# Kernel optimization log

Measured on AMD Instinct MI355X. Metric: run time of the kernel, lower is better.

## Reference

```python
import math
import jax, jax.numpy as jnp
import numpy as np

D_MODEL = 512
H = 8          # head_num
HD = 64        # head_dim
ETA = 4
R = 8
D_FFC = 2048
EPS = 1e-6
GRU_BIAS = 2.0
T, B = 128, 32
TOTAL_PROJ = H * HD * 5 + H * ETA * 3  # 2656


def _layer_norm(x, g, b):
    m = x.mean(-1, keepdims=True)
    v = ((x - m) ** 2).mean(-1, keepdims=True)
    return (x - m) / jnp.sqrt(v + 1e-5) * g + b


def _outer(a, b):
    # a: (T,B,H,D), b: (T,B,H,E) -> (T,B,H,D*E), row-major over (D,E) like torch bmm+reshape
    t, bb, h, d = a.shape
    return (a[..., :, None] * b[..., None, :]).reshape(t, bb, h, d * b.shape[-1])


def _gru_gate(x, y, w, u):
    # GTrXL-style gating: x = residual stream, y = new signal. w,u: (3, d, d)
    r = jax.nn.sigmoid(y @ w[0].T + x @ u[0].T)
    z = jax.nn.sigmoid(y @ w[1].T + x @ u[1].T - GRU_BIAS)
    h = jnp.tanh(y @ w[2].T + (r * x) @ u[2].T)
    return (1.0 - z) * x + z * h


def _discounted_sum(prev, x, d):
    # y_t = d_t * y_{t-1} + x_t, y_{-1} = prev. x: (T, ...), d broadcastable to x.
    def step(c, xd):
        xi, di = xd
        nc = di * c + xi
        return nc, nc
    _, ys = jax.lax.scan(step, prev, (x, d))
    return ys


def setup_inputs() -> dict:
    key = jax.random.key(0)
    ks = jax.random.split(key, 12)
    sc_p = 1.0 / math.sqrt(D_MODEL)
    return {
        "inputs": jax.random.normal(ks[0], (T, B, D_MODEL), jnp.float32),
        "terminations": jax.random.randint(ks[1], (T, B), 0, 2).astype(jnp.int32),
        "tilde_k": jnp.zeros((B, R, H, ETA * HD), jnp.float32),
        "tilde_v": jnp.zeros((B, R, H, HD), jnp.float32),
        "s_prev": jnp.zeros((B, H, ETA * HD), jnp.float32),
        "tick": jnp.zeros((B, 1), jnp.float32),
        "w_proj": jax.random.normal(ks[2], (TOTAL_PROJ, D_MODEL), jnp.float32) * sc_p,
        "b_proj": jnp.zeros((TOTAL_PROJ,), jnp.float32),
        "w_attn": jax.random.normal(ks[3], (D_MODEL, H * HD), jnp.float32) * (1.0 / math.sqrt(H * HD)),
        "b_attn": jnp.zeros((D_MODEL,), jnp.float32),
        "ln1_g": jnp.ones((D_MODEL,), jnp.float32),
        "ln1_b": jnp.zeros((D_MODEL,), jnp.float32),
        "ln2_g": jnp.ones((D_MODEL,), jnp.float32),
        "ln2_b": jnp.zeros((D_MODEL,), jnp.float32),
        "gru1_w": jax.random.normal(ks[4], (3, D_MODEL, D_MODEL), jnp.float32) * sc_p,
        "gru1_u": jax.random.normal(ks[5], (3, D_MODEL, D_MODEL), jnp.float32) * sc_p,
        "gru2_w": jax.random.normal(ks[6], (3, D_MODEL, D_MODEL), jnp.float32) * sc_p,
        "gru2_u": jax.random.normal(ks[7], (3, D_MODEL, D_MODEL), jnp.float32) * sc_p,
        "ffc_w1": jax.random.normal(ks[8], (D_FFC, D_MODEL), jnp.float32) * sc_p,
        "ffc_b1": jnp.zeros((D_FFC,), jnp.float32),
        "ffc_w2": jax.random.normal(ks[9], (D_MODEL, D_FFC), jnp.float32) * (1.0 / math.sqrt(D_FFC)),
        "ffc_b2": jnp.zeros((D_MODEL,), jnp.float32),
    }


def _forward(inputs, terminations, tilde_k, tilde_v, s_prev, tick,
             w_proj, b_proj, w_attn, b_attn, ln1_g, ln1_b, ln2_g, ln2_b,
             gru1_w, gru1_u, gru2_w, gru2_u, ffc_w1, ffc_b1, ffc_w2, ffc_b2):
    t, bsz, _ = inputs.shape
    omegas = jnp.linspace(-math.pi, math.pi, R).astype(inputs.dtype)

    x_normed = _layer_norm(inputs, ln1_g, ln1_b)
    all_proj = x_normed @ w_proj.T + b_proj  # (T,B,2656)
    kqv_dim = H * HD * 5
    kqvbg = all_proj[..., :kqv_dim].reshape(t, bsz, H, 5, HD)
    p123 = all_proj[..., kqv_dim:].reshape(t, bsz, H, 3, ETA)

    keys = kqvbg[..., 0, :]
    queries = kqvbg[..., 1, :]
    values = kqvbg[..., 2, :]
    beta = jax.nn.sigmoid(kqvbg[..., 3, :])
    gammas = kqvbg[..., 4, :]
    p1, p2, p3 = p123[..., 0, :], p123[..., 1, :], p123[..., 2, :]

    keys_exp = _outer(jax.nn.relu(keys), jax.nn.relu(p1))          # (T,B,H,HD*ETA)
    queries_exp = _outer(jax.nn.relu(queries), jax.nn.relu(p2))
    gammas_exp = _outer(jax.nn.sigmoid(gammas), jax.nn.sigmoid(p3))

    ticks = tick[None] + jnp.arange(1, t + 1, dtype=tick.dtype).reshape(t, 1, 1)  # (T,B,1)
    occil = jnp.cos(ticks * omegas)  # (T,B,R)

    values_gated = values * beta                 # (T,B,H,HD)
    keys_gated = keys_exp * gammas_exp           # (T,B,H,HD*ETA)
    s_in = keys_gated
    values_osc = values_gated[:, :, None] * occil[..., None, None]  # (T,B,R,H,HD)
    keys_osc = keys_gated[:, :, None] * occil[..., None, None]      # (T,B,R,H,HD*ETA)

    term_mask = (1.0 - terminations.astype(inputs.dtype))[:, :, None, None]  # (T,B,1,1)
    discount_gamma = (1.0 - gammas_exp) * term_mask   # (T,B,H,HD*ETA)
    discount_beta = (1.0 - beta) * term_mask          # (T,B,H,HD)

    final_keys = _discounted_sum(tilde_k, keys_osc, discount_gamma[:, :, None])
    final_values = _discounted_sum(tilde_v, values_osc, discount_beta[:, :, None])
    final_s = _discounted_sum(s_prev, s_in, discount_gamma)

    kdq = (final_keys * queries_exp[:, :, None]).sum(-1)   # (T,B,R,H)
    kv = (final_values * kdq[..., None]).sum(2)             # (T,B,H,HD)
    norm = (final_s * queries_exp).sum(-1) + EPS            # (T,B,H)
    attn = kv / (2 * R * norm[..., None])
    attn = attn.reshape(t, bsz, H * HD) @ w_attn.T + b_attn  # (T,B,d_model)

    gating1 = _gru_gate(inputs, jax.nn.relu(attn), gru1_w, gru1_u)
    ffc_in = _layer_norm(gating1, ln2_g, ln2_b)
    ffc_out = jax.nn.relu(jax.nn.relu(ffc_in @ ffc_w1.T + ffc_b1) @ ffc_w2.T + ffc_b2)
    output = _gru_gate(gating1, ffc_out, gru2_w, gru2_u)
    return output


def reference(inputs, terminations, tilde_k, tilde_v, s_prev, tick,
              w_proj, b_proj, w_attn, b_attn, ln1_g, ln1_b, ln2_g, ln2_b,
              gru1_w, gru1_u, gru2_w, gru2_u, ffc_w1, ffc_b1, ffc_w2, ffc_b2):
    return _forward(inputs, terminations, tilde_k, tilde_v, s_prev, tick,
                    w_proj, b_proj, w_attn, b_attn, ln1_g, ln1_b, ln2_g, ln2_b,
                    gru1_w, gru1_u, gru2_w, gru2_u, ffc_w1, ffc_b1, ffc_w2, ffc_b2)
```

## Files before the change

### kernel.cpp

```cpp
#include <hip/hip_runtime.h>
#include <hip/hip_bf16.h>
#include <math.h>

#define DM   512
#define HH   8
#define RR   8
#define TT   128
#define BBATCH 32
#define MM   (TT*BBATCH)
#define NPROJ 2656
#define KQV  2560

typedef __attribute__((ext_vector_type(8))) short bf16x8;
typedef __attribute__((ext_vector_type(4))) float f32x4;

__device__ __forceinline__ float sigmoidf_(float x) {
    return 1.0f / (1.0f + __expf(-x));
}

__device__ __forceinline__ void gload_lds16(const void* g, void* l) {
    __builtin_amdgcn_global_load_lds(
        (const __attribute__((address_space(1))) unsigned int*)g,
        (__attribute__((address_space(3))) unsigned int*)l, 16, 0, 0);
}

template<int CTRL, int RMASK>
__device__ __forceinline__ float dpp_add_(float x) {
    union { float f; int i; } a, b;
    a.f = x;
    b.i = __builtin_amdgcn_update_dpp(0, a.i, CTRL, RMASK, 0xf, true);
    return x + b.f;
}
__device__ __forceinline__ float wave_sum_u(float x) {
    x = dpp_add_<0x111, 0xf>(x);
    x = dpp_add_<0x112, 0xf>(x);
    x = dpp_add_<0x114, 0xf>(x);
    x = dpp_add_<0x118, 0xf>(x);
    x = dpp_add_<0x142, 0xa>(x);
    x = dpp_add_<0x143, 0xc>(x);
    union { float f; int i; } s, t;
    s.f = x;
    t.i = __builtin_amdgcn_readlane(s.i, 63);
    return t.f;
}

struct F2B9 {
    const float* s[9];
    __hip_bfloat16* d[9];
    int cum[10];
};

__global__ __launch_bounds__(256) void f2b_ln_all(F2B9 a,
    const float* __restrict__ x, const float* __restrict__ g,
    const float* __restrict__ b, __hip_bfloat16* __restrict__ lnout)
{
    if (blockIdx.x < 8752) {
        int q = blockIdx.x * 256 + threadIdx.x;
        if (q >= a.cum[9]) return;
        int s = 0;
        #pragma unroll
        for (int i = 1; i < 9; ++i) s += (q >= a.cum[i]);
        int i4 = (q - a.cum[s]) * 4;
        float4 v = *(const float4*)(a.s[s] + i4);
        __hip_bfloat16* dst = a.d[s] + i4;
        dst[0] = __float2bfloat16(v.x);
        dst[1] = __float2bfloat16(v.y);
        dst[2] = __float2bfloat16(v.z);
        dst[3] = __float2bfloat16(v.w);
        return;
    }
    int row = blockIdx.x - 8752;
    int tid = threadIdx.x;
    const float* xr = x + (size_t)row * DM;
    float2 v = ((const float2*)xr)[tid];
    float s = v.x + v.y;
    #pragma unroll
    for (int off = 32; off; off >>= 1) s += __shfl_down(s, off);
    __shared__ float red[8];
    int wid = tid >> 6, lane = tid & 63;
    if (lane == 0) red[wid] = s;
    __syncthreads();
    if (tid == 0) red[0] = (red[0] + red[1] + red[2] + red[3]) * (1.0f / DM);
    __syncthreads();
    float mean = red[0];
    float dx = v.x - mean, dy = v.y - mean;
    float sq = dx*dx + dy*dy;
    #pragma unroll
    for (int off = 32; off; off >>= 1) sq += __shfl_down(sq, off);
    if (lane == 0) red[4 + wid] = sq;
    __syncthreads();
    if (tid == 0) red[1] = rsqrtf((red[4]+red[5]+red[6]+red[7]) * (1.0f/DM) + 1e-5f);
    __syncthreads();
    float rstd = red[1];
    float2 gg = ((const float2*)g)[tid];
    float2 bb = ((const float2*)b)[tid];
    __hip_bfloat16* orow = lnout + (size_t)row * DM;
    orow[2*tid+0] = __float2bfloat16(dx * rstd * gg.x + bb.x);
    orow[2*tid+1] = __float2bfloat16(dy * rstd * gg.y + bb.y);
}

__device__ __forceinline__ void gemm_core128(
    const __hip_bfloat16* __restrict__ A, const __hip_bfloat16* __restrict__ W,
    const float* __restrict__ bias,
    float* __restrict__ Cf, __hip_bfloat16* __restrict__ Cb,
    int N, int K, int act, int m0, int n0,
    __hip_bfloat16* As, __hip_bfloat16* Bs)
{
    int tid = threadIdx.x;
    int wave = tid >> 6, lane = tid & 63;
    int wm = (wave >> 1) * 64, wn = (wave & 1) * 64;
    int fr = lane & 15, fq = lane >> 4;

    f32x4 acc[4][4];
    #pragma unroll
    for (int i = 0; i < 4; ++i)
        #pragma unroll
        for (int j = 0; j < 4; ++j)
            acc[i][j] = (f32x4){0.f, 0.f, 0.f, 0.f};

    int sm0 = wave*16 + fr;
    int sm1 = sm0 + 64;
    int wr0 = n0 + sm0; if (wr0 >= N) wr0 = N - 1;
    int wr1 = n0 + sm1; if (wr1 >= N) wr1 = N - 1;
    const __hip_bfloat16* Ag0 = A + (size_t)(m0 + sm0) * K + fq*8;
    const __hip_bfloat16* Ag1 = A + (size_t)(m0 + sm1) * K + fq*8;
    const __hip_bfloat16* Wg0 = W + (size_t)wr0 * K + fq*8;
    const __hip_bfloat16* Wg1 = W + (size_t)wr1 * K + fq*8;

    for (int k0 = 0; k0 < K; k0 += 32) {
        gload_lds16(Ag0 + k0, As + (size_t)wave*512);
        gload_lds16(Ag1 + k0, As + (size_t)(wave+4)*512);
        gload_lds16(Wg0 + k0, Bs + (size_t)wave*512);
        gload_lds16(Wg1 + k0, Bs + (size_t)(wave+4)*512);
        __syncthreads();
        bf16x8 af[4], bfr[4];
        #pragma unroll
        for (int i = 0; i < 4; ++i) {
            af[i]  = *(const bf16x8*)(As + (size_t)(wm/16 + i)*512 + lane*8);
            bfr[i] = *(const bf16x8*)(Bs + (size_t)(wn/16 + i)*512 + lane*8);
        }
        #pragma unroll
        for (int mi = 0; mi < 4; ++mi)
            #pragma unroll
            for (int ni = 0; ni < 4; ++ni)
                acc[mi][ni] = __builtin_amdgcn_mfma_f32_16x16x32_bf16(
                    af[mi], bfr[ni], acc[mi][ni], 0, 0, 0);
        __syncthreads();
    }

    #pragma unroll
    for (int ni = 0; ni < 4; ++ni) {
        int n = n0 + wn + ni*16 + fr;
        bool nok = n < N;
        float bv = (bias && nok) ? bias[n] : 0.f;
        #pragma unroll
        for (int mi = 0; mi < 4; ++mi) {
            #pragma unroll
            for (int r = 0; r < 4; ++r) {
                int m = m0 + wm + mi*16 + fq*4 + r;
                float v = acc[mi][ni][r] + bv;
                if (act) v = fmaxf(v, 0.f);
                if (nok) {
                    size_t idx = (size_t)m * N + n;
                    if (Cf) Cf[idx] = v;
                    if (Cb) Cb[idx] = __float2bfloat16(v);
                }
            }
        }
    }
}

__global__ __launch_bounds__(256) void gemm_bf16(
    const __hip_bfloat16* __restrict__ A, const __hip_bfloat16* __restrict__ W,
    const float* __restrict__ bias,
    float* __restrict__ Cf, __hip_bfloat16* __restrict__ Cb,
    int N, int K, int act)
{
    __shared__ __attribute__((aligned(16))) __hip_bfloat16 As[8*512];
    __shared__ __attribute__((aligned(16))) __hip_bfloat16 Bs[8*512];
    gemm_core128(A, W, bias, Cf, Cb, N, K, act, blockIdx.y * 128, blockIdx.x * 128, As, Bs);
}

__global__ __launch_bounds__(256) void ffc1_bx_dual(
    const __hip_bfloat16* __restrict__ Aa, const __hip_bfloat16* __restrict__ Wa,
    const float* __restrict__ biasA, __hip_bfloat16* __restrict__ CbA,
    int Na, int splitX,
    const __hip_bfloat16* __restrict__ Ab, const __hip_bfloat16* __restrict__ Wb,
    float* __restrict__ CfB, int Nb, int K)
{
    __shared__ __attribute__((aligned(16))) __hip_bfloat16 As[8*512];
    __shared__ __attribute__((aligned(16))) __hip_bfloat16 Bs[8*512];
    int bx = blockIdx.x;
    if (bx < splitX)
        gemm_core128(Aa, Wa, biasA, nullptr, CbA, Na, K, 1, blockIdx.y*128, bx*128, As, Bs);
    else
        gemm_core128(Ab, Wb, nullptr, CfB, nullptr, Nb, K, 0, blockIdx.y*128, (bx-splitX)*128, As, Bs);
}

__global__ __launch_bounds__(256) void gemm_bf16_64(
    const __hip_bfloat16* __restrict__ A, const __hip_bfloat16* __restrict__ W,
    const float* __restrict__ bias,
    float* __restrict__ Cf, __hip_bfloat16* __restrict__ Cb,
    int N, int K, int act)
{
    __shared__ __attribute__((aligned(16))) __hip_bfloat16 As[4*512];
    __shared__ __attribute__((aligned(16))) __hip_bfloat16 Bs[8*512];
    int tid = threadIdx.x;
    int wave = tid >> 6, lane = tid & 63;
    int m0 = blockIdx.y * 64, n0 = blockIdx.x * 128;
    int wm = (wave >> 1) * 32, wn = (wave & 1) * 64;
    int fr = lane & 15, fq = lane >> 4;

    f32x4 acc[2][4];
    #pragma unroll
    for (int i = 0; i < 2; ++i)
        #pragma unroll
        for (int j = 0; j < 4; ++j)
            acc[i][j] = (f32x4){0.f, 0.f, 0.f, 0.f};

    const __hip_bfloat16* Ag = A + (size_t)(m0 + wave*16 + fr) * K + fq*8;
    int wr0 = n0 + wave*16 + fr; if (wr0 >= N) wr0 = N - 1;
    int wr1 = wr0 + 64;          if (wr1 >= N) wr1 = N - 1;
    const __hip_bfloat16* Wg0 = W + (size_t)wr0 * K + fq*8;
    const __hip_bfloat16* Wg1 = W + (size_t)wr1 * K + fq*8;

    for (int k0 = 0; k0 < K; k0 += 32) {
        gload_lds16(Ag  + k0, As + (size_t)wave*512);
        gload_lds16(Wg0 + k0, Bs + (size_t)wave*512);
        gload_lds16(Wg1 + k0, Bs + (size_t)(wave+4)*512);
        __syncthreads();
        bf16x8 af[2], bfr[4];
        #pragma unroll
        for (int i = 0; i < 2; ++i)
            af[i]  = *(const bf16x8*)(As + (size_t)(wm/16 + i)*512 + lane*8);
        #pragma unroll
        for (int j = 0; j < 4; ++j)
            bfr[j] = *(const bf16x8*)(Bs + (size_t)(wn/16 + j)*512 + lane*8);
        #pragma unroll
        for (int mi = 0; mi < 2; ++mi)
            #pragma unroll
            for (int ni = 0; ni < 4; ++ni)
                acc[mi][ni] = __builtin_amdgcn_mfma_f32_16x16x32_bf16(
                    af[mi], bfr[ni], acc[mi][ni], 0, 0, 0);
        __syncthreads();
    }

    #pragma unroll
    for (int ni = 0; ni < 4; ++ni) {
        int n = n0 + wn + ni*16 + fr;
        bool nok = n < N;
        float bv = (bias && nok) ? bias[n] : 0.f;
        #pragma unroll
        for (int mi = 0; mi < 2; ++mi) {
            #pragma unroll
            for (int r = 0; r < 4; ++r) {
                int m = m0 + wm + mi*16 + fq*4 + r;
                float v = acc[mi][ni][r] + bv;
                if (act) v = fmaxf(v, 0.f);
                if (nok) {
                    size_t idx = (size_t)m * N + n;
                    if (Cf) Cf[idx] = v;
                    if (Cb) Cb[idx] = __float2bfloat16(v);
                }
            }
        }
    }
}

#define NCH   4
#define CHK   32
#define BNDF  (44*64)

__global__ __launch_bounds__(256) void scan_attn_fused(
    const float* __restrict__ proj, const int* __restrict__ term,
    const float* __restrict__ tick, const float* __restrict__ tilde_k,
    const float* __restrict__ tilde_v, const float* __restrict__ s_prev,
    __hip_bfloat16* __restrict__ attn,
    const __hip_bfloat16* __restrict__ gA, const __hip_bfloat16* __restrict__ gW,
    float* __restrict__ gC)
{
    extern __shared__ __attribute__((aligned(16))) char smem_dyn[];
    int bid = blockIdx.x;
    if (bid >= 256) {
        __hip_bfloat16* As = (__hip_bfloat16*)smem_dyn;
        __hip_bfloat16* Bs = As + 8*512;
        int g = bid - 256;
        gemm_core128(gA, gW, nullptr, gC, nullptr, 1024, DM, 0,
                     (g >> 3) * 128, (g & 7) * 128, As, Bs);
        return;
    }

    float* bnd  = (float*)smem_dyn;
    float* occt = bnd + 3*BNDF;
    int*   flags= (int*)(occt + TT*8);

    const int b = bid >> 3, h = bid & 7;
    const int tid = threadIdx.x;
    const int wv = tid >> 6, lane = tid & 63;
    const int t0 = wv * CHK;

    const float tk = tick[b];
    if (tid < 4) flags[tid] = 0;
    {
        const float PI_ = 3.14159265358979323846f;
        #pragma unroll
        for (int i = 0; i < 4; ++i) {
            int idx = tid*4 + i;
            int t = idx >> 3, r = idx & 7;
            float w = -PI_ + (float)r * (2.0f*PI_/7.0f);
            occt[idx] = cosf((tk + (float)(t + 1)) * w);
        }
    }
    __syncthreads();

    int tmv = (lane < CHK) ? term[(size_t)(t0 + lane)*BBATCH + b] : 0;

    float fs[4], fk[8][4], fv[8], Pg[4], Pb;

    auto zero_state = [&]() {
        #pragma unroll
        for (int j = 0; j < 4; ++j) fs[j] = 0.f;
        #pragma unroll
        for (int r = 0; r < 8; ++r) {
            #pragma unroll
            for (int j = 0; j < 4; ++j) fk[r][j] = 0.f;
            fv[r] = 0.f;
        }
    };
    auto load_init = [&]() {
        float4 s4 = *(const float4*)(s_prev + ((size_t)(b*HH + h))*256 + lane*4);
        fs[0]=s4.x; fs[1]=s4.y; fs[2]=s4.z; fs[3]=s4.w;
        #pragma unroll
        for (int r = 0; r < 8; ++r) {
            float4 k4 = *(const float4*)(tilde_k + (((size_t)b*RR + r)*HH + h)*256 + lane*4);
            fk[r][0]=k4.x; fk[r][1]=k4.y; fk[r][2]=k4.z; fk[r][3]=k4.w;
            fv[r] = tilde_v[(((size_t)b*RR + r)*HH + h)*64 + lane];
        }
    };
    auto load_bnd = [&](int w) {
        const float* p = bnd + w*BNDF;
        #pragma unroll
        for (int j = 0; j < 4; ++j) fs[j] = p[j*64 + lane];
        #pragma unroll
        for (int r = 0; r < 8; ++r) {
            #pragma unroll
            for (int j = 0; j < 4; ++j) fk[r][j] = p[(4 + r*4 + j)*64 + lane];
            fv[r] = p[(36 + r)*64 + lane];
        }
    };
    auto store_bnd = [&](int w) {
        float* p = bnd + w*BNDF;
        #pragma unroll
        for (int j = 0; j < 4; ++j) p[j*64 + lane] = fs[j];
        #pragma unroll
        for (int r = 0; r < 8; ++r) {
            #pragma unroll
            for (int j = 0; j < 4; ++j) p[(4 + r*4 + j)*64 + lane] = fk[r][j];
            p[(36 + r)*64 + lane] = fv[r];
        }
    };
    auto combine = [&](int w) {
        const float* p = bnd + w*BNDF;
        #pragma unroll
        for (int j = 0; j < 4; ++j) fs[j] = fmaf(Pg[j], p[j*64 + lane], fs[j]);
        #pragma unroll
        for (int r = 0; r < 8; ++r) {
            #pragma unroll
            for (int j = 0; j < 4; ++j)
                fk[r][j] = fmaf(Pg[j], p[(4 + r*4 + j)*64 + lane], fk[r][j]);
            fv[r] = fmaf(Pb, p[(36 + r)*64 + lane], fv[r]);
        }
    };

    struct Raw { float k, q, v, be, ga; float4 P1, P2, P3; };
    auto load_raw = [&](int t, Raw& rw) {
        const float* prow = proj + (size_t)(t*BBATCH + b) * NPROJ;
        const float* p5 = prow + h*320;
        rw.k  = p5[lane];
        rw.q  = p5[64  + lane];
        rw.v  = p5[128 + lane];
        rw.be = p5[192 + lane];
        rw.ga = p5[256 + lane];
        const float* pp = prow + KQV + h*12;
        rw.P1 = *(const float4*)(pp);
        rw.P2 = *(const float4*)(pp + 4);
        rw.P3 = *(const float4*)(pp + 8);
    };

    auto sweep = [&](bool out) {
        Pg[0]=Pg[1]=Pg[2]=Pg[3]=1.f; Pb=1.f;
        Raw cur, nxt;
        load_raw(t0, cur);
        for (int i = 0; i < CHK; ++i) {
            const int t = t0 + i;
            if (i + 1 < CHK) load_raw(t + 1, nxt);
            const int tm = __builtin_amdgcn_readlane(tmv, i);
            const float mask = 1.0f - (float)tm;
            float kr = fmaxf(cur.k, 0.f);
            float sg = sigmoidf_(cur.ga);
            float sb = sigmoidf_(cur.be);
            float vg = cur.v * sb;
            float db = (1.f - sb) * mask;
            float p1a[4] = {cur.P1.x, cur.P1.y, cur.P1.z, cur.P1.w};
            float p3a[4] = {cur.P3.x, cur.P3.y, cur.P3.z, cur.P3.w};
            float kg[4], dg[4];
            #pragma unroll
            for (int j = 0; j < 4; ++j) {
                float gexp = sg * sigmoidf_(p3a[j]);
                kg[j] = kr * fmaxf(p1a[j], 0.f) * gexp;
                dg[j] = (1.f - gexp) * mask;
            }
            float occ[8];
            {
                float4 o0 = *(const float4*)(occt + t*8);
                float4 o1 = *(const float4*)(occt + t*8 + 4);
                occ[0]=o0.x; occ[1]=o0.y; occ[2]=o0.z; occ[3]=o0.w;
                occ[4]=o1.x; occ[5]=o1.y; occ[6]=o1.z; occ[7]=o1.w;
            }
            #pragma unroll
            for (int j = 0; j < 4; ++j) {
                fs[j] = fmaf(dg[j], fs[j], kg[j]);
                Pg[j] *= dg[j];
            }
            #pragma unroll
            for (int r = 0; r < 8; ++r) {
                #pragma unroll
                for (int j = 0; j < 4; ++j)
                    fk[r][j] = fmaf(dg[j], fk[r][j], kg[j]*occ[r]);
                fv[r] = fmaf(db, fv[r], vg*occ[r]);
            }
            Pb *= db;
            if (out) {
                float qr = fmaxf(cur.q, 0.f);
                float p2a[4] = {cur.P2.x, cur.P2.y, cur.P2.z, cur.P2.w};
                float qe[4];
                #pragma unroll
                for (int j = 0; j < 4; ++j) qe[j] = qr * fmaxf(p2a[j], 0.f);
                float snorm = fs[0]*qe[0] + fs[1]*qe[1] + fs[2]*qe[2] + fs[3]*qe[3];
                float nrm_u = wave_sum_u(snorm);
                float kdq_u[8];
                #pragma unroll
                for (int r = 0; r < 8; ++r) {
                    float kdq = fk[r][0]*qe[0] + fk[r][1]*qe[1]
                              + fk[r][2]*qe[2] + fk[r][3]*qe[3];
                    kdq_u[r] = wave_sum_u(kdq);
                }
                float kv = 0.f;
                #pragma unroll
                for (int r = 0; r < 8; ++r) kv = fmaf(fv[r], kdq_u[r], kv);
                attn[(size_t)(t*BBATCH + b)*DM + h*64 + lane] =
                    __float2bfloat16(kv / (16.f * (nrm_u + 1e-6f)));
            }
            cur = nxt;
        }
    };

    if (wv < NCH - 1) {
        if (wv == 0) load_init(); else zero_state();
        sweep(false);
        if (wv > 0) {
            while (__hip_atomic_load(&flags[wv-1], __ATOMIC_ACQUIRE,
                                     __HIP_MEMORY_SCOPE_WORKGROUP) == 0)
                __builtin_amdgcn_s_sleep(1);
            combine(wv - 1);
        }
        store_bnd(wv);
        if (lane == 0)
            __hip_atomic_store(&flags[wv], 1, __ATOMIC_RELEASE,
                               __HIP_MEMORY_SCOPE_WORKGROUP);
    }

    if (wv == 0) {
        load_init();
    } else {
        while (__hip_atomic_load(&flags[wv-1], __ATOMIC_ACQUIRE,
                                 __HIP_MEMORY_SCOPE_WORKGROUP) == 0)
            __builtin_amdgcn_s_sleep(1);
        load_bnd(wv - 1);
    }
    sweep(true);
}

__global__ __launch_bounds__(256) void gru_rz_kernel(const float* __restrict__ A1,
    const float* __restrict__ Bx, const float* __restrict__ x,
    __hip_bfloat16* __restrict__ rx, float* __restrict__ z)
{
    size_t i = (size_t)blockIdx.x * 256 + threadIdx.x;
    size_t m = i >> 9;
    int c = (int)(i & 511);
    float rpre = A1[m*1536 + c]       + Bx[m*1024 + c];
    float zpre = A1[m*1536 + 512 + c] + Bx[m*1024 + 512 + c] - 2.0f;
    rx[i] = __float2bfloat16(sigmoidf_(rpre) * x[i]);
    z[i]  = sigmoidf_(zpre);
}

__global__ __launch_bounds__(256) void gru_final_kernel(const float* __restrict__ A1,
    const float* __restrict__ C2, const float* __restrict__ z,
    const float* __restrict__ x, float* __restrict__ out)
{
    size_t i = (size_t)blockIdx.x * 256 + threadIdx.x;
    size_t m = i >> 9;
    int c = (int)(i & 511);
    float hh = tanhf(A1[m*1536 + 1024 + c] + C2[i]);
    float zz = z[i];
    out[i] = (1.0f - zz) * x[i] + zz * hh;
}

__global__ __launch_bounds__(256) void gru_final_ln(
    const float* __restrict__ A1, const float* __restrict__ C2,
    const float* __restrict__ z, const float* __restrict__ x,
    const float* __restrict__ g, const float* __restrict__ bta,
    float* __restrict__ g1, __hip_bfloat16* __restrict__ g1b,
    __hip_bfloat16* __restrict__ fib)
{
    int row = blockIdx.x;
    int tid = threadIdx.x;
    size_t base = (size_t)row * DM;
    float2 c2v = ((const float2*)(C2 + base))[tid];
    float2 zv  = ((const float2*)(z  + base))[tid];
    float2 xv  = ((const float2*)(x  + base))[tid];
    float2 av  = ((const float2*)(A1 + (size_t)row*1536 + 1024))[tid];
    float h0 = tanhf(av.x + c2v.x);
    float h1 = tanhf(av.y + c2v.y);
    float2 v;
    v.x = (1.0f - zv.x) * xv.x + zv.x * h0;
    v.y = (1.0f - zv.y) * xv.y + zv.y * h1;
    ((float2*)(g1 + base))[tid] = v;
    g1b[base + 2*tid+0] = __float2bfloat16(v.x);
    g1b[base + 2*tid+1] = __float2bfloat16(v.y);

    float s = v.x + v.y;
    #pragma unroll
    for (int off = 32; off; off >>= 1) s += __shfl_down(s, off);
    __shared__ float red[8];
    int wid = tid >> 6, lane = tid & 63;
    if (lane == 0) red[wid] = s;
    __syncthreads();
    if (tid == 0) red[0] = (red[0] + red[1] + red[2] + red[3]) * (1.0f / DM);
    __syncthreads();
    float mean = red[0];
    float dx = v.x - mean, dy = v.y - mean;
    float sq = dx*dx + dy*dy;
    #pragma unroll
    for (int off = 32; off; off >>= 1) sq += __shfl_down(sq, off);
    if (lane == 0) red[4 + wid] = sq;
    __syncthreads();
    if (tid == 0) red[1] = rsqrtf((red[4]+red[5]+red[6]+red[7]) * (1.0f/DM) + 1e-5f);
    __syncthreads();
    float rstd = red[1];
    float2 gg = ((const float2*)g)[tid];
    float2 bb = ((const float2*)bta)[tid];
    fib[base + 2*tid+0] = __float2bfloat16(dx * rstd * gg.x + bb.x);
    fib[base + 2*tid+1] = __float2bfloat16(dy * rstd * gg.y + bb.y);
}

extern "C" void kernel_launch(void* const* d_in, const int* in_sizes, int n_in,
                              void* d_out, int out_size, void* d_ws, size_t ws_size,
                              hipStream_t stream)
{
    const float* inputs = (const float*)d_in[0];
    const int*   term   = (const int*)  d_in[1];
    const float* tilde_k= (const float*)d_in[2];
    const float* tilde_v= (const float*)d_in[3];
    const float* s_prev = (const float*)d_in[4];
    const float* tick   = (const float*)d_in[5];
    const float* w_proj = (const float*)d_in[6];
    const float* b_proj = (const float*)d_in[7];
    const float* w_attn = (const float*)d_in[8];
    const float* b_attn = (const float*)d_in[9];
    const float* ln1_g  = (const float*)d_in[10];
    const float* ln1_b  = (const float*)d_in[11];
    const float* ln2_g  = (const float*)d_in[12];
    const float* ln2_b  = (const float*)d_in[13];
    const float* gru1_w = (const float*)d_in[14];
    const float* gru1_u = (const float*)d_in[15];
    const float* gru2_w = (const float*)d_in[16];
    const float* gru2_u = (const float*)d_in[17];
    const float* ffc_w1 = (const float*)d_in[18];
    const float* ffc_b1 = (const float*)d_in[19];
    const float* ffc_w2 = (const float*)d_in[20];
    const float* ffc_b2 = (const float*)d_in[21];
    float* out = (float*)d_out;
    float* ws  = (float*)d_ws;

    float* proj = ws;
    float* A1   = ws;
    float* C2   = ws + 10878976;
    float* zb   = ws + 12976128;
    float* g1   = ws + 15073280;
    __hip_bfloat16* bb = (__hip_bfloat16*)(ws + 17170432);
    __hip_bfloat16* wp_bf  = bb + 0;
    __hip_bfloat16* wat_bf = bb + 1359872;
    __hip_bfloat16* g1w_bf = bb + 1622016;
    __hip_bfloat16* g1u_bf = bb + 2408448;
    __hip_bfloat16* g2w_bf = bb + 3194880;
    __hip_bfloat16* g2u_bf = bb + 3981312;
    __hip_bfloat16* fw1_bf = bb + 4767744;
    __hip_bfloat16* fw2_bf = bb + 5816320;
    __hip_bfloat16* in_bf  = bb + 6864896;
    __hip_bfloat16* xn_bf  = bb + 8962048;
    __hip_bfloat16* at_bf  = bb + 11059200;
    __hip_bfloat16* y1_bf  = bb + 13156352;
    __hip_bfloat16* rx_bf  = bb + 15253504;
    __hip_bfloat16* fi_bf  = bb + 17350656;
    __hip_bfloat16* mid_bf = bb + 19447808;
    __hip_bfloat16* fo_bf  = bb + 27836416;
    __hip_bfloat16* g1_bf  = bb + 29933568;
    float* Bx = ws + 33185792;

    dim3 blk(256);

    F2B9 fa;
    const float* srcs[9] = {w_proj, w_attn, gru1_w, gru1_u, gru2_w, gru2_u,
                            ffc_w1, ffc_w2, inputs};
    __hip_bfloat16* dsts[9] = {wp_bf, wat_bf, g1w_bf, g1u_bf, g2w_bf, g2u_bf,
                               fw1_bf, fw2_bf, in_bf};
    int quads[9] = {339968, 65536, 196608, 196608, 196608, 196608,
                    262144, 262144, 524288};
    int cum = 0;
    for (int i = 0; i < 9; ++i) { fa.s[i] = srcs[i]; fa.d[i] = dsts[i]; fa.cum[i] = cum; cum += quads[i]; }
    fa.cum[9] = cum;
    f2b_ln_all<<<8752 + MM, blk, 0, stream>>>(fa, inputs, ln1_g, ln1_b, xn_bf);

    gemm_bf16<<<dim3(21, 32), blk, 0, stream>>>(xn_bf, wp_bf, b_proj, proj, nullptr, NPROJ, DM, 0);

    size_t dyn = (size_t)(3*BNDF + TT*8 + 4) * 4;
    scan_attn_fused<<<512, blk, dyn, stream>>>(proj, term, tick, tilde_k, tilde_v,
                                               s_prev, at_bf, in_bf, g1u_bf, Bx);

    gemm_bf16_64<<<dim3(4, 64), blk, 0, stream>>>(at_bf, wat_bf, b_attn, nullptr, y1_bf, DM, DM, 1);

    gemm_bf16<<<dim3(12, 32), blk, 0, stream>>>(y1_bf, g1w_bf, nullptr, A1, nullptr, 3*DM, DM, 0);
    gru_rz_kernel<<<MM*DM/256, blk, 0, stream>>>(A1, Bx, inputs, rx_bf, zb);
    gemm_bf16_64<<<dim3(4, 64), blk, 0, stream>>>(rx_bf, g1u_bf + 2*DM*DM, nullptr, C2, nullptr, DM, DM, 0);
    gru_final_ln<<<MM, blk, 0, stream>>>(A1, C2, zb, inputs, ln2_g, ln2_b, g1, g1_bf, fi_bf);

    ffc1_bx_dual<<<dim3(24, 32), blk, 0, stream>>>(fi_bf, fw1_bf, ffc_b1, mid_bf,
                                                   2048, 16,
                                                   g1_bf, g2u_bf, Bx, 1024, DM);

    gemm_bf16_64<<<dim3(4, 64), blk, 0, stream>>>(mid_bf, fw2_bf, ffc_b2, nullptr, fo_bf, DM, 2048, 1);

    gemm_bf16<<<dim3(12, 32), blk, 0, stream>>>(fo_bf, g2w_bf, nullptr, A1, nullptr, 3*DM, DM, 0);
    gru_rz_kernel<<<MM*DM/256, blk, 0, stream>>>(A1, Bx, g1, rx_bf, zb);
    gemm_bf16_64<<<dim3(4, 64), blk, 0, stream>>>(rx_bf, g2u_bf + 2*DM*DM, nullptr, C2, nullptr, DM, DM, 0);
    gru_final_kernel<<<MM*DM/256, blk, 0, stream>>>(A1, C2, zb, g1, out);
}
```

Measured before the change: 408.6 us.

## Fuse GRU gate elementwise ops into GEMM epilogues and widen scan chunking

GEMM bodies are templated on an epilogue functor, so the GRU r/z sigmoid and the final tanh blend run inside the GEMM write-out and the separate elementwise kernels disappear. This removes the round trip of the full 3*DM A1 and C2 intermediates through memory. The scan kernel moves to 512 threads with 8 chunks of 16 timesteps, using a chained double-buffered boundary handoff so each wave does one partial sweep, one combine and one final sweep. The Bx side-GEMM gets a dedicated 2-wave-tile variant. The LayerNorm formerly fused with the GRU final step becomes a standalone kernel, which adds a re-read of g1.

```diff
diff --git a/kernel.cpp b/kernel.cpp
--- a/kernel.cpp
+++ b/kernel.cpp
@@ -99,12 +99,45 @@
     orow[2*tid+1] = __float2bfloat16(dy * rstd * gg.y + bb.y);
 }
 
-__device__ __forceinline__ void gemm_core128(
+__global__ __launch_bounds__(256) void ln_kernel(const float* __restrict__ x,
+    const float* __restrict__ g, const float* __restrict__ b,
+    __hip_bfloat16* __restrict__ out)
+{
+    int row = blockIdx.x;
+    int tid = threadIdx.x;
+    const float* xr = x + (size_t)row * DM;
+    float2 v = ((const float2*)xr)[tid];
+    float s = v.x + v.y;
+    #pragma unroll
+    for (int off = 32; off; off >>= 1) s += __shfl_down(s, off);
+    __shared__ float red[8];
+    int wid = tid >> 6, lane = tid & 63;
+    if (lane == 0) red[wid] = s;
+    __syncthreads();
+    if (tid == 0) red[0] = (red[0] + red[1] + red[2] + red[3]) * (1.0f / DM);
+    __syncthreads();
+    float mean = red[0];
+    float dx = v.x - mean, dy = v.y - mean;
+    float sq = dx*dx + dy*dy;
+    #pragma unroll
+    for (int off = 32; off; off >>= 1) sq += __shfl_down(sq, off);
+    if (lane == 0) red[4 + wid] = sq;
+    __syncthreads();
+    if (tid == 0) red[1] = rsqrtf((red[4]+red[5]+red[6]+red[7]) * (1.0f/DM) + 1e-5f);
+    __syncthreads();
+    float rstd = red[1];
+    float2 gg = ((const float2*)g)[tid];
+    float2 bb = ((const float2*)b)[tid];
+    __hip_bfloat16* orow = out + (size_t)row * DM;
+    orow[2*tid+0] = __float2bfloat16(dx * rstd * gg.x + bb.x);
+    orow[2*tid+1] = __float2bfloat16(dy * rstd * gg.y + bb.y);
+}
+
+template<class Epi>
+__device__ __forceinline__ void gemm128_body(
     const __hip_bfloat16* __restrict__ A, const __hip_bfloat16* __restrict__ W,
-    const float* __restrict__ bias,
-    float* __restrict__ Cf, __hip_bfloat16* __restrict__ Cb,
-    int N, int K, int act, int m0, int n0,
-    __hip_bfloat16* As, __hip_bfloat16* Bs)
+    int N, int K, int m0, int n0,
+    __hip_bfloat16* As, __hip_bfloat16* Bs, Epi epi)
 {
     int tid = threadIdx.x;
     int wave = tid >> 6, lane = tid & 63;
@@ -151,20 +184,128 @@
     #pragma unroll
     for (int ni = 0; ni < 4; ++ni) {
         int n = n0 + wn + ni*16 + fr;
-        bool nok = n < N;
-        float bv = (bias && nok) ? bias[n] : 0.f;
+        if (n >= N) continue;
         #pragma unroll
         for (int mi = 0; mi < 4; ++mi) {
             #pragma unroll
             for (int r = 0; r < 4; ++r) {
                 int m = m0 + wm + mi*16 + fq*4 + r;
-                float v = acc[mi][ni][r] + bv;
-                if (act) v = fmaxf(v, 0.f);
-                if (nok) {
-                    size_t idx = (size_t)m * N + n;
-                    if (Cf) Cf[idx] = v;
-                    if (Cb) Cb[idx] = __float2bfloat16(v);
-                }
+                epi(m, n, acc[mi][ni][r]);
+            }
+        }
+    }
+}
+
+template<class Epi>
+__device__ __forceinline__ void gemm64_body(
+    const __hip_bfloat16* __restrict__ A, const __hip_bfloat16* __restrict__ W,
+    int N, int K, int m0, int n0,
+    __hip_bfloat16* As, __hip_bfloat16* Bs, Epi epi)
+{
+    int tid = threadIdx.x;
+    int wave = tid >> 6, lane = tid & 63;
+    int wm = (wave >> 1) * 32, wn = (wave & 1) * 64;
+    int fr = lane & 15, fq = lane >> 4;
+
+    f32x4 acc[2][4];
+    #pragma unroll
+    for (int i = 0; i < 2; ++i)
+        #pragma unroll
+        for (int j = 0; j < 4; ++j)
+            acc[i][j] = (f32x4){0.f, 0.f, 0.f, 0.f};
+
+    const __hip_bfloat16* Ag = A + (size_t)(m0 + wave*16 + fr) * K + fq*8;
+    int wr0 = n0 + wave*16 + fr; if (wr0 >= N) wr0 = N - 1;
+    int wr1 = wr0 + 64;          if (wr1 >= N) wr1 = N - 1;
+    const __hip_bfloat16* Wg0 = W + (size_t)wr0 * K + fq*8;
+    const __hip_bfloat16* Wg1 = W + (size_t)wr1 * K + fq*8;
+
+    for (int k0 = 0; k0 < K; k0 += 32) {
+        gload_lds16(Ag  + k0, As + (size_t)wave*512);
+        gload_lds16(Wg0 + k0, Bs + (size_t)wave*512);
+        gload_lds16(Wg1 + k0, Bs + (size_t)(wave+4)*512);
+        __syncthreads();
+        bf16x8 af[2], bfr[4];
+        #pragma unroll
+        for (int i = 0; i < 2; ++i)
+            af[i]  = *(const bf16x8*)(As + (size_t)(wm/16 + i)*512 + lane*8);
+        #pragma unroll
+        for (int j = 0; j < 4; ++j)
+            bfr[j] = *(const bf16x8*)(Bs + (size_t)(wn/16 + j)*512 + lane*8);
+        #pragma unroll
+        for (int mi = 0; mi < 2; ++mi)
+            #pragma unroll
+            for (int ni = 0; ni < 4; ++ni)
+                acc[mi][ni] = __builtin_amdgcn_mfma_f32_16x16x32_bf16(
+                    af[mi], bfr[ni], acc[mi][ni], 0, 0, 0);
+        __syncthreads();
+    }
+
+    #pragma unroll
+    for (int ni = 0; ni < 4; ++ni) {
+        int n = n0 + wn + ni*16 + fr;
+        if (n >= N) continue;
+        #pragma unroll
+        for (int mi = 0; mi < 2; ++mi) {
+            #pragma unroll
+            for (int r = 0; r < 4; ++r) {
+                int m = m0 + wm + mi*16 + fq*4 + r;
+                epi(m, n, acc[mi][ni][r]);
+            }
+        }
+    }
+}
+
+__device__ __forceinline__ void gemm_bx_w8(
+    const __hip_bfloat16* __restrict__ A, const __hip_bfloat16* __restrict__ W,
+    float* __restrict__ Cf, int N, int K, int m0, int n0,
+    __hip_bfloat16* As, __hip_bfloat16* Bs)
+{
+    int tid = threadIdx.x;
+    int wave = tid >> 6, lane = tid & 63;
+    int wm = (wave >> 1) * 32, wn = (wave & 1) * 64;
+    int fr = lane & 15, fq = lane >> 4;
+
+    f32x4 acc[2][4];
+    #pragma unroll
+    for (int i = 0; i < 2; ++i)
+        #pragma unroll
+        for (int j = 0; j < 4; ++j)
+            acc[i][j] = (f32x4){0.f, 0.f, 0.f, 0.f};
+
+    int sm = wave*16 + fr;
+    const __hip_bfloat16* Ag = A + (size_t)(m0 + sm) * K + fq*8;
+    const __hip_bfloat16* Wg = W + (size_t)(n0 + sm) * K + fq*8;
+
+    for (int k0 = 0; k0 < K; k0 += 32) {
+        gload_lds16(Ag + k0, As + (size_t)wave*512);
+        gload_lds16(Wg + k0, Bs + (size_t)wave*512);
+        __syncthreads();
+        bf16x8 af[2], bfr[4];
+        #pragma unroll
+        for (int i = 0; i < 2; ++i)
+            af[i]  = *(const bf16x8*)(As + (size_t)(wm/16 + i)*512 + lane*8);
+        #pragma unroll
+        for (int j = 0; j < 4; ++j)
+            bfr[j] = *(const bf16x8*)(Bs + (size_t)(wn/16 + j)*512 + lane*8);
+        #pragma unroll
+        for (int mi = 0; mi < 2; ++mi)
+            #pragma unroll
+            for (int ni = 0; ni < 4; ++ni)
+                acc[mi][ni] = __builtin_amdgcn_mfma_f32_16x16x32_bf16(
+                    af[mi], bfr[ni], acc[mi][ni], 0, 0, 0);
+        __syncthreads();
+    }
+
+    #pragma unroll
+    for (int ni = 0; ni < 4; ++ni) {
+        int n = n0 + wn + ni*16 + fr;
+        #pragma unroll
+        for (int mi = 0; mi < 2; ++mi) {
+            #pragma unroll
+            for (int r = 0; r < 4; ++r) {
+                int m = m0 + wm + mi*16 + fq*4 + r;
+                Cf[(size_t)m * N + n] = acc[mi][ni][r];
             }
         }
     }
@@ -178,7 +319,14 @@
 {
     __shared__ __attribute__((aligned(16))) __hip_bfloat16 As[8*512];
     __shared__ __attribute__((aligned(16))) __hip_bfloat16 Bs[8*512];
-    gemm_core128(A, W, bias, Cf, Cb, N, K, act, blockIdx.y * 128, blockIdx.x * 128, As, Bs);
+    gemm128_body(A, W, N, K, blockIdx.y * 128, blockIdx.x * 128, As, Bs,
+        [&](int m, int n, float v) {
+            float vv = v + (bias ? bias[n] : 0.f);
+            if (act) vv = fmaxf(vv, 0.f);
+            size_t idx = (size_t)m * N + n;
+            if (Cf) Cf[idx] = vv;
+            if (Cb) Cb[idx] = __float2bfloat16(vv);
+        });
 }
 
 __global__ __launch_bounds__(256) void ffc1_bx_dual(
@@ -191,10 +339,18 @@
     __shared__ __attribute__((aligned(16))) __hip_bfloat16 As[8*512];
     __shared__ __attribute__((aligned(16))) __hip_bfloat16 Bs[8*512];
     int bx = blockIdx.x;
-    if (bx < splitX)
-        gemm_core128(Aa, Wa, biasA, nullptr, CbA, Na, K, 1, blockIdx.y*128, bx*128, As, Bs);
-    else
-        gemm_core128(Ab, Wb, nullptr, CfB, nullptr, Nb, K, 0, blockIdx.y*128, (bx-splitX)*128, As, Bs);
+    if (bx < splitX) {
+        gemm128_body(Aa, Wa, Na, K, blockIdx.y*128, bx*128, As, Bs,
+            [&](int m, int n, float v) {
+                float vv = fmaxf(v + biasA[n], 0.f);
+                CbA[(size_t)m * Na + n] = __float2bfloat16(vv);
+            });
+    } else {
+        gemm128_body(Ab, Wb, Nb, K, blockIdx.y*128, (bx-splitX)*128, As, Bs,
+            [&](int m, int n, float v) {
+                CfB[(size_t)m * Nb + n] = v;
+            });
+    }
 }
 
 __global__ __launch_bounds__(256) void gemm_bf16_64(
@@ -205,73 +361,63 @@
 {
     __shared__ __attribute__((aligned(16))) __hip_bfloat16 As[4*512];
     __shared__ __attribute__((aligned(16))) __hip_bfloat16 Bs[8*512];
-    int tid = threadIdx.x;
-    int wave = tid >> 6, lane = tid & 63;
-    int m0 = blockIdx.y * 64, n0 = blockIdx.x * 128;
-    int wm = (wave >> 1) * 32, wn = (wave & 1) * 64;
-    int fr = lane & 15, fq = lane >> 4;
-
-    f32x4 acc[2][4];
-    #pragma unroll
-    for (int i = 0; i < 2; ++i)
-        #pragma unroll
-        for (int j = 0; j < 4; ++j)
-            acc[i][j] = (f32x4){0.f, 0.f, 0.f, 0.f};
-
-    const __hip_bfloat16* Ag = A + (size_t)(m0 + wave*16 + fr) * K + fq*8;
-    int wr0 = n0 + wave*16 + fr; if (wr0 >= N) wr0 = N - 1;
-    int wr1 = wr0 + 64;          if (wr1 >= N) wr1 = N - 1;
-    const __hip_bfloat16* Wg0 = W + (size_t)wr0 * K + fq*8;
-    const __hip_bfloat16* Wg1 = W + (size_t)wr1 * K + fq*8;
-
-    for (int k0 = 0; k0 < K; k0 += 32) {
-        gload_lds16(Ag  + k0, As + (size_t)wave*512);
-        gload_lds16(Wg0 + k0, Bs + (size_t)wave*512);
-        gload_lds16(Wg1 + k0, Bs + (size_t)(wave+4)*512);
-        __syncthreads();
-        bf16x8 af[2], bfr[4];
-        #pragma unroll
-        for (int i = 0; i < 2; ++i)
-            af[i]  = *(const bf16x8*)(As + (size_t)(wm/16 + i)*512 + lane*8);
-        #pragma unroll
-        for (int j = 0; j < 4; ++j)
-            bfr[j] = *(const bf16x8*)(Bs + (size_t)(wn/16 + j)*512 + lane*8);
-        #pragma unroll
-        for (int mi = 0; mi < 2; ++mi)
-            #pragma unroll
-            for (int ni = 0; ni < 4; ++ni)
-                acc[mi][ni] = __builtin_amdgcn_mfma_f32_16x16x32_bf16(
-                    af[mi], bfr[ni], acc[mi][ni], 0, 0, 0);
-        __syncthreads();
-    }
-
-    #pragma unroll
-    for (int ni = 0; ni < 4; ++ni) {
-        int n = n0 + wn + ni*16 + fr;
-        bool nok = n < N;
-        float bv = (bias && nok) ? bias[n] : 0.f;
-        #pragma unroll
-        for (int mi = 0; mi < 2; ++mi) {
-            #pragma unroll
-            for (int r = 0; r < 4; ++r) {
-                int m = m0 + wm + mi*16 + fq*4 + r;
-                float v = acc[mi][ni][r] + bv;
-                if (act) v = fmaxf(v, 0.f);
-                if (nok) {
-                    size_t idx = (size_t)m * N + n;
-                    if (Cf) Cf[idx] = v;
-                    if (Cb) Cb[idx] = __float2bfloat16(v);
-                }
-            }
-        }
-    }
-}
-
-#define NCH   4
-#define CHK   32
+    gemm64_body(A, W, N, K, blockIdx.y * 64, blockIdx.x * 128, As, Bs,
+        [&](int m, int n, float v) {
+            float vv = v + (bias ? bias[n] : 0.f);
+            if (act) vv = fmaxf(vv, 0.f);
+            size_t idx = (size_t)m * N + n;
+            if (Cf) Cf[idx] = vv;
+            if (Cb) Cb[idx] = __float2bfloat16(vv);
+        });
+}
+
+__global__ __launch_bounds__(256) void gemm_gruA(
+    const __hip_bfloat16* __restrict__ A, const __hip_bfloat16* __restrict__ W,
+    const float* __restrict__ Bx, const float* __restrict__ x,
+    __hip_bfloat16* __restrict__ rx, float* __restrict__ z,
+    float* __restrict__ A1h)
+{
+    __shared__ __attribute__((aligned(16))) __hip_bfloat16 As[8*512];
+    __shared__ __attribute__((aligned(16))) __hip_bfloat16 Bs[8*512];
+    gemm128_body(A, W, 3*DM, DM, blockIdx.y * 128, blockIdx.x * 128, As, Bs,
+        [&](int m, int n, float v) {
+            size_t mb = (size_t)m;
+            if (n < 512) {
+                float rpre = v + Bx[mb*1024 + n];
+                rx[mb*512 + n] = __float2bfloat16(sigmoidf_(rpre) * x[mb*512 + n]);
+            } else if (n < 1024) {
+                float zpre = v + Bx[mb*1024 + n] - 2.0f;
+                z[mb*512 + (n - 512)] = sigmoidf_(zpre);
+            } else {
+                A1h[mb*512 + (n - 1024)] = v;
+            }
+        });
+}
+
+__global__ __launch_bounds__(256) void gemm_gruC(
+    const __hip_bfloat16* __restrict__ A, const __hip_bfloat16* __restrict__ W,
+    const float* __restrict__ A1h, const float* __restrict__ z,
+    const float* __restrict__ x,
+    float* __restrict__ outF, __hip_bfloat16* __restrict__ outB)
+{
+    __shared__ __attribute__((aligned(16))) __hip_bfloat16 As[4*512];
+    __shared__ __attribute__((aligned(16))) __hip_bfloat16 Bs[8*512];
+    gemm64_body(A, W, DM, DM, blockIdx.y * 64, blockIdx.x * 128, As, Bs,
+        [&](int m, int n, float v) {
+            size_t i = (size_t)m * 512 + n;
+            float hh = tanhf(A1h[i] + v);
+            float zz = z[i];
+            float o = (1.0f - zz) * x[i] + zz * hh;
+            outF[i] = o;
+            if (outB) outB[i] = __float2bfloat16(o);
+        });
+}
+
+#define NCH   8
+#define CHK   16
 #define BNDF  (44*64)
 
-__global__ __launch_bounds__(256) void scan_attn_fused(
+__global__ __launch_bounds__(512) void scan_attn_fused(
     const float* __restrict__ proj, const int* __restrict__ term,
     const float* __restrict__ tick, const float* __restrict__ tilde_k,
     const float* __restrict__ tilde_v, const float* __restrict__ s_prev,
@@ -285,13 +431,12 @@
         __hip_bfloat16* As = (__hip_bfloat16*)smem_dyn;
         __hip_bfloat16* Bs = As + 8*512;
         int g = bid - 256;
-        gemm_core128(gA, gW, nullptr, gC, nullptr, 1024, DM, 0,
-                     (g >> 3) * 128, (g & 7) * 128, As, Bs);
+        gemm_bx_w8(gA, gW, gC, 1024, DM, (g >> 3) * 128, (g & 7) * 128, As, Bs);
         return;
     }
 
     float* bnd  = (float*)smem_dyn;
-    float* occt = bnd + 3*BNDF;
+    float* occt = bnd + 2*BNDF;
     int*   flags= (int*)(occt + TT*8);
 
     const int b = bid >> 3, h = bid & 7;
@@ -300,12 +445,12 @@
     const int t0 = wv * CHK;
 
     const float tk = tick[b];
-    if (tid < 4) flags[tid] = 0;
+    if (tid < 8) flags[tid] = 0;
     {
         const float PI_ = 3.14159265358979323846f;
         #pragma unroll
-        for (int i = 0; i < 4; ++i) {
-            int idx = tid*4 + i;
+        for (int i = 0; i < 2; ++i) {
+            int idx = tid*2 + i;
             int t = idx >> 3, r = idx & 7;
             float w = -PI_ + (float)r * (2.0f*PI_/7.0f);
             occt[idx] = cosf((tk + (float)(t + 1)) * w);
@@ -316,6 +461,7 @@
     int tmv = (lane < CHK) ? term[(size_t)(t0 + lane)*BBATCH + b] : 0;
 
     float fs[4], fk[8][4], fv[8], Pg[4], Pb;
+    float is_[4], ik[8][4], iv[8];
 
     auto zero_state = [&]() {
         #pragma unroll
@@ -329,27 +475,37 @@
     };
     auto load_init = [&]() {
         float4 s4 = *(const float4*)(s_prev + ((size_t)(b*HH + h))*256 + lane*4);
-        fs[0]=s4.x; fs[1]=s4.y; fs[2]=s4.z; fs[3]=s4.w;
+        is_[0]=s4.x; is_[1]=s4.y; is_[2]=s4.z; is_[3]=s4.w;
         #pragma unroll
         for (int r = 0; r < 8; ++r) {
             float4 k4 = *(const float4*)(tilde_k + (((size_t)b*RR + r)*HH + h)*256 + lane*4);
-            fk[r][0]=k4.x; fk[r][1]=k4.y; fk[r][2]=k4.z; fk[r][3]=k4.w;
-            fv[r] = tilde_v[(((size_t)b*RR + r)*HH + h)*64 + lane];
+            ik[r][0]=k4.x; ik[r][1]=k4.y; ik[r][2]=k4.z; ik[r][3]=k4.w;
+            iv[r] = tilde_v[(((size_t)b*RR + r)*HH + h)*64 + lane];
         }
     };
-    auto load_bnd = [&](int w) {
-        const float* p = bnd + w*BNDF;
-        #pragma unroll
-        for (int j = 0; j < 4; ++j) fs[j] = p[j*64 + lane];
+    auto state_from_init = [&]() {
+        #pragma unroll
+        for (int j = 0; j < 4; ++j) fs[j] = is_[j];
         #pragma unroll
         for (int r = 0; r < 8; ++r) {
             #pragma unroll
-            for (int j = 0; j < 4; ++j) fk[r][j] = p[(4 + r*4 + j)*64 + lane];
-            fv[r] = p[(36 + r)*64 + lane];
+            for (int j = 0; j < 4; ++j) fk[r][j] = ik[r][j];
+            fv[r] = iv[r];
         }
     };
-    auto store_bnd = [&](int w) {
-        float* p = bnd + w*BNDF;
+    auto read_bnd = [&](int slot) {
+        const float* p = bnd + slot*BNDF;
+        #pragma unroll
+        for (int j = 0; j < 4; ++j) is_[j] = p[j*64 + lane];
+        #pragma unroll
+        for (int r = 0; r < 8; ++r) {
+            #pragma unroll
+            for (int j = 0; j < 4; ++j) ik[r][j] = p[(4 + r*4 + j)*64 + lane];
+            iv[r] = p[(36 + r)*64 + lane];
+        }
+    };
+    auto store_bnd = [&](int slot) {
+        float* p = bnd + slot*BNDF;
         #pragma unroll
         for (int j = 0; j < 4; ++j) p[j*64 + lane] = fs[j];
         #pragma unroll
@@ -359,16 +515,15 @@
             p[(36 + r)*64 + lane] = fv[r];
         }
     };
-    auto combine = [&](int w) {
-        const float* p = bnd + w*BNDF;
-        #pragma unroll
-        for (int j = 0; j < 4; ++j) fs[j] = fmaf(Pg[j], p[j*64 + lane], fs[j]);
+    auto combine = [&]() {
+        #pragma unroll
+        for (int j = 0; j < 4; ++j) fs[j] = fmaf(Pg[j], is_[j], fs[j]);
         #pragma unroll
         for (int r = 0; r < 8; ++r) {
             #pragma unroll
             for (int j = 0; j < 4; ++j)
-                fk[r][j] = fmaf(Pg[j], p[(4 + r*4 + j)*64 + lane], fk[r][j]);
-            fv[r] = fmaf(Pb, p[(36 + r)*64 + lane], fv[r]);
+                fk[r][j] = fmaf(Pg[j], ik[r][j], fk[r][j]);
+            fv[r] = fmaf(Pb, iv[r], fv[r]);
         }
     };
 
@@ -455,103 +610,32 @@
         }
     };
 
+    if (wv == 0) {
+        load_init();
+        state_from_init();
+        sweep(true);
+        store_bnd(0);
+        if (lane == 0)
+            __hip_atomic_store(&flags[0], 1, __ATOMIC_RELEASE,
+                               __HIP_MEMORY_SCOPE_WORKGROUP);
+        return;
+    }
+
+    zero_state();
+    sweep(false);
+    while (__hip_atomic_load(&flags[wv-1], __ATOMIC_ACQUIRE,
+                             __HIP_MEMORY_SCOPE_WORKGROUP) == 0)
+        __builtin_amdgcn_s_sleep(1);
+    read_bnd((wv-1) & 1);
+    combine();
     if (wv < NCH - 1) {
-        if (wv == 0) load_init(); else zero_state();
-        sweep(false);
-        if (wv > 0) {
-            while (__hip_atomic_load(&flags[wv-1], __ATOMIC_ACQUIRE,
-                                     __HIP_MEMORY_SCOPE_WORKGROUP) == 0)
-                __builtin_amdgcn_s_sleep(1);
-            combine(wv - 1);
-        }
-        store_bnd(wv);
+        store_bnd(wv & 1);
         if (lane == 0)
             __hip_atomic_store(&flags[wv], 1, __ATOMIC_RELEASE,
                                __HIP_MEMORY_SCOPE_WORKGROUP);
     }
-
-    if (wv == 0) {
-        load_init();
-    } else {
-        while (__hip_atomic_load(&flags[wv-1], __ATOMIC_ACQUIRE,
-                                 __HIP_MEMORY_SCOPE_WORKGROUP) == 0)
-            __builtin_amdgcn_s_sleep(1);
-        load_bnd(wv - 1);
-    }
+    state_from_init();
     sweep(true);
-}
-
-__global__ __launch_bounds__(256) void gru_rz_kernel(const float* __restrict__ A1,
-    const float* __restrict__ Bx, const float* __restrict__ x,
-    __hip_bfloat16* __restrict__ rx, float* __restrict__ z)
-{
-    size_t i = (size_t)blockIdx.x * 256 + threadIdx.x;
-    size_t m = i >> 9;
-    int c = (int)(i & 511);
-    float rpre = A1[m*1536 + c]       + Bx[m*1024 + c];
-    float zpre = A1[m*1536 + 512 + c] + Bx[m*1024 + 512 + c] - 2.0f;
-    rx[i] = __float2bfloat16(sigmoidf_(rpre) * x[i]);
-    z[i]  = sigmoidf_(zpre);
-}
-
-__global__ __launch_bounds__(256) void gru_final_kernel(const float* __restrict__ A1,
-    const float* __restrict__ C2, const float* __restrict__ z,
-    const float* __restrict__ x, float* __restrict__ out)
-{
-    size_t i = (size_t)blockIdx.x * 256 + threadIdx.x;
-    size_t m = i >> 9;
-    int c = (int)(i & 511);
-    float hh = tanhf(A1[m*1536 + 1024 + c] + C2[i]);
-    float zz = z[i];
-    out[i] = (1.0f - zz) * x[i] + zz * hh;
-}
-
-__global__ __launch_bounds__(256) void gru_final_ln(
-    const float* __restrict__ A1, const float* __restrict__ C2,
-    const float* __restrict__ z, const float* __restrict__ x,
-    const float* __restrict__ g, const float* __restrict__ bta,
-    float* __restrict__ g1, __hip_bfloat16* __restrict__ g1b,
-    __hip_bfloat16* __restrict__ fib)
-{
-    int row = blockIdx.x;
-    int tid = threadIdx.x;
-    size_t base = (size_t)row * DM;
-    float2 c2v = ((const float2*)(C2 + base))[tid];
-    float2 zv  = ((const float2*)(z  + base))[tid];
-    float2 xv  = ((const float2*)(x  + base))[tid];
-    float2 av  = ((const float2*)(A1 + (size_t)row*1536 + 1024))[tid];
-    float h0 = tanhf(av.x + c2v.x);
-    float h1 = tanhf(av.y + c2v.y);
-    float2 v;
-    v.x = (1.0f - zv.x) * xv.x + zv.x * h0;
-    v.y = (1.0f - zv.y) * xv.y + zv.y * h1;
-    ((float2*)(g1 + base))[tid] = v;
-    g1b[base + 2*tid+0] = __float2bfloat16(v.x);
-    g1b[base + 2*tid+1] = __float2bfloat16(v.y);
-
-    float s = v.x + v.y;
-    #pragma unroll
-    for (int off = 32; off; off >>= 1) s += __shfl_down(s, off);
-    __shared__ float red[8];
-    int wid = tid >> 6, lane = tid & 63;
-    if (lane == 0) red[wid] = s;
-    __syncthreads();
-    if (tid == 0) red[0] = (red[0] + red[1] + red[2] + red[3]) * (1.0f / DM);
-    __syncthreads();
-    float mean = red[0];
-    float dx = v.x - mean, dy = v.y - mean;
-    float sq = dx*dx + dy*dy;
-    #pragma unroll
-    for (int off = 32; off; off >>= 1) sq += __shfl_down(sq, off);
-    if (lane == 0) red[4 + wid] = sq;
-    __syncthreads();
-    if (tid == 0) red[1] = rsqrtf((red[4]+red[5]+red[6]+red[7]) * (1.0f/DM) + 1e-5f);
-    __syncthreads();
-    float rstd = red[1];
-    float2 gg = ((const float2*)g)[tid];
-    float2 bb = ((const float2*)bta)[tid];
-    fib[base + 2*tid+0] = __float2bfloat16(dx * rstd * gg.x + bb.x);
-    fib[base + 2*tid+1] = __float2bfloat16(dy * rstd * gg.y + bb.y);
 }
 
 extern "C" void kernel_launch(void* const* d_in, const int* in_sizes, int n_in,
@@ -584,8 +668,7 @@
     float* ws  = (float*)d_ws;
 
     float* proj = ws;
-    float* A1   = ws;
-    float* C2   = ws + 10878976;
+    float* A1h  = ws;
     float* zb   = ws + 12976128;
     float* g1   = ws + 15073280;
     __hip_bfloat16* bb = (__hip_bfloat16*)(ws + 17170432);
@@ -624,16 +707,15 @@
 
     gemm_bf16<<<dim3(21, 32), blk, 0, stream>>>(xn_bf, wp_bf, b_proj, proj, nullptr, NPROJ, DM, 0);
 
-    size_t dyn = (size_t)(3*BNDF + TT*8 + 4) * 4;
-    scan_attn_fused<<<512, blk, dyn, stream>>>(proj, term, tick, tilde_k, tilde_v,
-                                               s_prev, at_bf, in_bf, g1u_bf, Bx);
+    size_t dyn = (size_t)(2*BNDF + TT*8 + 16) * 4;
+    scan_attn_fused<<<512, dim3(512), dyn, stream>>>(proj, term, tick, tilde_k, tilde_v,
+                                                     s_prev, at_bf, in_bf, g1u_bf, Bx);
 
     gemm_bf16_64<<<dim3(4, 64), blk, 0, stream>>>(at_bf, wat_bf, b_attn, nullptr, y1_bf, DM, DM, 1);
 
-    gemm_bf16<<<dim3(12, 32), blk, 0, stream>>>(y1_bf, g1w_bf, nullptr, A1, nullptr, 3*DM, DM, 0);
-    gru_rz_kernel<<<MM*DM/256, blk, 0, stream>>>(A1, Bx, inputs, rx_bf, zb);
-    gemm_bf16_64<<<dim3(4, 64), blk, 0, stream>>>(rx_bf, g1u_bf + 2*DM*DM, nullptr, C2, nullptr, DM, DM, 0);
-    gru_final_ln<<<MM, blk, 0, stream>>>(A1, C2, zb, inputs, ln2_g, ln2_b, g1, g1_bf, fi_bf);
+    gemm_gruA<<<dim3(12, 32), blk, 0, stream>>>(y1_bf, g1w_bf, Bx, inputs, rx_bf, zb, A1h);
+    gemm_gruC<<<dim3(4, 64), blk, 0, stream>>>(rx_bf, g1u_bf + 2*DM*DM, A1h, zb, inputs, g1, g1_bf);
+    ln_kernel<<<MM, blk, 0, stream>>>(g1, ln2_g, ln2_b, fi_bf);
 
     ffc1_bx_dual<<<dim3(24, 32), blk, 0, stream>>>(fi_bf, fw1_bf, ffc_b1, mid_bf,
                                                    2048, 16,
@@ -641,8 +723,6 @@
 
     gemm_bf16_64<<<dim3(4, 64), blk, 0, stream>>>(mid_bf, fw2_bf, ffc_b2, nullptr, fo_bf, DM, 2048, 1);
 
-    gemm_bf16<<<dim3(12, 32), blk, 0, stream>>>(fo_bf, g2w_bf, nullptr, A1, nullptr, 3*DM, DM, 0);
-    gru_rz_kernel<<<MM*DM/256, blk, 0, stream>>>(A1, Bx, g1, rx_bf, zb);
-    gemm_bf16_64<<<dim3(4, 64), blk, 0, stream>>>(rx_bf, g2u_bf + 2*DM*DM, nullptr, C2, nullptr, DM, DM, 0);
-    gru_final_kernel<<<MM*DM/256, blk, 0, stream>>>(A1, C2, zb, g1, out);
-}
+    gemm_gruA<<<dim3(12, 32), blk, 0, stream>>>(fo_bf, g2w_bf, Bx, g1, rx_bf, zb, A1h);
+    gemm_gruC<<<dim3(4, 64), blk, 0, stream>>>(rx_bf, g2u_bf + 2*DM*DM, A1h, zb, g1, out, nullptr);
+}
```

Measured after the change: 473.0 us. 15.8% more time.
